# Kernel tuning notes

Measured on AMD Instinct MI355X. Metric: run time of the kernel, lower is better.

Reference implementation:

```python
import jax, jax.numpy as jnp
import numpy as np

IN, H, OUT = 128, 256, 128


def setup_inputs() -> dict:
    key = jax.random.key(0)
    ks = jax.random.split(key, 12)
    B, T = 32, 128
    s_in = 1.0 / np.sqrt(IN)
    s_h = 1.0 / np.sqrt(H)
    return {
        "x": jax.random.normal(ks[0], (B, T, IN), dtype=jnp.float32),
        "timespans": jax.random.uniform(ks[1], (B, T), dtype=jnp.float32),
        "tau_sys": jax.random.uniform(ks[2], (H,), dtype=jnp.float32) * 10.0 + 1.0,
        "sigma": jnp.ones((H,), dtype=jnp.float32) * 0.5,
        "W_A": jax.random.normal(ks[3], (H, H), dtype=jnp.float32) * s_h,
        "W_B": jax.random.normal(ks[4], (H, IN), dtype=jnp.float32) * s_in,
        "b_B": jax.random.normal(ks[5], (H,), dtype=jnp.float32) * s_in,
        "W_C": jax.random.normal(ks[6], (OUT, H), dtype=jnp.float32) * s_h,
        "b_C": jax.random.normal(ks[7], (OUT,), dtype=jnp.float32) * s_h,
        "W_ih": jax.random.normal(ks[8], (4 * H, IN), dtype=jnp.float32) * s_h,
        "W_hh": jax.random.normal(ks[9], (4 * H, H), dtype=jnp.float32) * s_h,
        "b_ih": jax.random.normal(ks[10], (4 * H,), dtype=jnp.float32) * s_h,
        "b_hh": jax.random.normal(ks[11], (4 * H,), dtype=jnp.float32) * s_h,
    }


def _lstm(x, W_ih, W_hh, b_ih, b_hh):
    # x: [B,T,IN] -> backbone_out: [B,T,H]; torch gate order i,f,g,o
    B = x.shape[0]
    xg = jnp.einsum("bti,gi->btg", x, W_ih) + b_ih  # precompute input contribution

    def step(carry, xg_t):
        h, c = carry
        gates = xg_t + h @ W_hh.T + b_hh
        i, f, g, o = jnp.split(gates, 4, axis=-1)
        c = jax.nn.sigmoid(f) * c + jax.nn.sigmoid(i) * jnp.tanh(g)
        h = jax.nn.sigmoid(o) * jnp.tanh(c)
        return (h, c), h

    h0 = jnp.zeros((B, H), dtype=x.dtype)
    c0 = jnp.zeros((B, H), dtype=x.dtype)
    _, hs = jax.lax.scan(step, (h0, c0), jnp.swapaxes(xg, 0, 1))
    return jnp.swapaxes(hs, 0, 1)  # [B,T,H]


def reference(x, timespans, tau_sys, sigma, W_A, W_B, b_B, W_C, b_C,
              W_ih, W_hh, b_ih, b_hh):
    B, T, _ = x.shape
    backbone_out = _lstm(x, W_ih, W_hh, b_ih, b_hh)  # [B,T,H]

    A_eff = W_A / tau_sys[None, :]        # [H,H] (divide columns, as in torch)
    I = jnp.eye(H, dtype=x.dtype)
    Bx = jnp.einsum("bti,hi->bth", x, W_B) + b_B  # precompute B(x_t) for all t

    def step(h, inp):
        x_t_Bx, bb_t, ts_t = inp  # [B,H], [B,H], [B]
        f_h = jnp.tanh(h / sigma)
        At = A_eff[None, :, :] * ts_t[:, None, None]            # [B,H,H]
        exp_At = I + At + 0.5 * jnp.einsum("bij,bjk->bik", At, At)
        h_new = jnp.einsum("bij,bj->bi", exp_At, h)
        drive = x_t_Bx + f_h @ W_A.T
        h_new = h_new + ts_t[:, None] * drive / tau_sys[None, :]
        h_new = h_new + bb_t
        y = h_new @ W_C.T + b_C
        return h_new, y

    h0 = jnp.zeros((B, H), dtype=x.dtype)
    xs = (jnp.swapaxes(Bx, 0, 1), jnp.swapaxes(backbone_out, 0, 1),
          jnp.swapaxes(timespans, 0, 1))
    _, ys = jax.lax.scan(step, h0, xs)
    return jnp.swapaxes(ys, 0, 1)  # [B,T,OUT]
```

## Files before the change

kernel.cpp:

```cpp
#include <hip/hip_runtime.h>
#include <math.h>

#define T_ 128

#define OFF_M2      0
#define OFF_WCOMBT  65536
#define OFF_BIAS    229376
#define OFF_WCT     230656
#define OFF_XG2     263424
#define OFF_BX2     4457728
#define OFF_HSEQ    5506304
#define OFF_HCSEQ   6554880

#define SENTB 0xFFFFFFFFu

__device__ __forceinline__ float sigm_f(float x) { return 1.0f / (1.0f + __expf(-x)); }
__device__ __forceinline__ float tanh_f(float x) { return 1.0f - 2.0f / (__expf(2.0f * x) + 1.0f); }

__device__ __forceinline__ unsigned long long aload_u64(const unsigned long long* p) {
  return __hip_atomic_load(p, __ATOMIC_RELAXED, __HIP_MEMORY_SCOPE_AGENT);
}
__device__ __forceinline__ void astore_f(float* p, float v) {
  __hip_atomic_store(p, v, __ATOMIC_RELAXED, __HIP_MEMORY_SCOPE_AGENT);
}
__device__ __forceinline__ bool bad_u64(unsigned long long v) {
  return (unsigned)v == SENTB || (unsigned)(v >> 32) == SENTB;
}

__global__ __launch_bounds__(256) void pack_kernel(
    const float* __restrict__ W_ih, const float* __restrict__ W_B,
    const float* __restrict__ b_ih, const float* __restrict__ b_hh,
    const float* __restrict__ b_B,  const float* __restrict__ W_C,
    float* __restrict__ ws) {
  int idx = blockIdx.x * 256 + threadIdx.x;
  if (idx < 163840) {
    int k = idx / 1280, c = idx - k * 1280;
    ws[OFF_WCOMBT + idx] = (c < 1024) ? W_ih[c * 128 + k] : W_B[(c - 1024) * 128 + k];
    return;
  }
  idx -= 163840;
  if (idx < 1280) {
    ws[OFF_BIAS + idx] = (idx < 1024) ? (b_ih[idx] + b_hh[idx]) : b_B[idx - 1024];
    return;
  }
  idx -= 1280;
  if (idx < 32768) {
    int k = idx >> 7, o = idx & 127;
    ws[OFF_WCT + idx] = W_C[o * 256 + k];
  }
}

__global__ __launch_bounds__(256) void m2_kernel(
    const float* __restrict__ W_A, const float* __restrict__ tau,
    float* __restrict__ M2) {
  __shared__ float adrow[256];
  const int i = blockIdx.x, k = threadIdx.x;
  const float itk = 1.0f / tau[k];
  adrow[k] = W_A[i * 256 + k] * itk;
  __syncthreads();
  float s = 0.f;
#pragma unroll 8
  for (int m = 0; m < 256; ++m)
    s = fmaf(adrow[m], W_A[m * 256 + k], s);
  M2[i * 256 + k] = s * itk;
}

__global__ __launch_bounds__(256) void xgt_kernel(
    const float* __restrict__ x, const float* __restrict__ WT,
    const float* __restrict__ bias, float* __restrict__ xg2,
    float* __restrict__ bx2) {
  __shared__ float xs[8 * 128];
  const int tid = threadIdx.x;
  const int rt = blockIdx.x, ct = blockIdx.y;
  ((float4*)xs)[tid] = ((const float4*)(x + rt * 1024))[tid];
  __syncthreads();
  const int r = tid >> 5, cg = tid & 31;
  const int c0 = ct * 256 + cg * 8;
  const float4* b4 = (const float4*)(bias + c0);
  float4 bA = b4[0], bB = b4[1];
  float a[8] = {bA.x, bA.y, bA.z, bA.w, bB.x, bB.y, bB.z, bB.w};
  const float4* xr4 = (const float4*)(xs + r * 128);
#pragma unroll 4
  for (int k4 = 0; k4 < 32; ++k4) {
    float4 xv = xr4[k4];
#define STEPB(kk, comp)                                                      \
    {                                                                        \
      const float4* w = (const float4*)(WT + (k4 * 4 + kk) * 1280 + c0);     \
      float4 wA = w[0], wB = w[1];                                           \
      a[0] = fmaf(wA.x, comp, a[0]); a[1] = fmaf(wA.y, comp, a[1]);          \
      a[2] = fmaf(wA.z, comp, a[2]); a[3] = fmaf(wA.w, comp, a[3]);          \
      a[4] = fmaf(wB.x, comp, a[4]); a[5] = fmaf(wB.y, comp, a[5]);          \
      a[6] = fmaf(wB.z, comp, a[6]); a[7] = fmaf(wB.w, comp, a[7]);          \
    }
    STEPB(0, xv.x) STEPB(1, xv.y) STEPB(2, xv.z) STEPB(3, xv.w)
#undef STEPB
  }
  const int row = rt * 8 + r;
  const int b = row >> 7, t = row & 127;
  if (ct < 4) {
    float* dst = xg2 + (size_t)(t * 32 + b) * 1024 + ct * 256 + cg * 8;
#pragma unroll
    for (int i = 0; i < 8; ++i) dst[i] = a[i];
  } else {
    float* dst = bx2 + (size_t)(t * 32 + b) * 256 + cg * 8;
#pragma unroll
    for (int i = 0; i < 8; ++i) dst[i] = a[i];
  }
}

__global__ __launch_bounds__(256) void recur_bp_kernel(
    const float* __restrict__ ts_all, const float* __restrict__ tau,
    const float* __restrict__ sigma, const float* __restrict__ W_hh,
    const float* __restrict__ W_A, const float* __restrict__ M2,
    const float* __restrict__ xg2, const float* __restrict__ bx2,
    float* __restrict__ hseq, float* __restrict__ hcseq) {
  const int tid = threadIdx.x;
  const int lane = tid & 63, w = tid >> 6;
  const unsigned long long* hsq  = (const unsigned long long*)hseq;
  const unsigned long long* hcsq = (const unsigned long long*)hcseq;

  __shared__ float h_s[2][256];
  __shared__ float q_s[2][768];

  if (blockIdx.x < 256) {
    const int b = blockIdx.x >> 3, cb = blockIdx.x & 7;
    const int p = lane >> 1, kh = lane & 1;
    const int gt = p >> 3, jj = p & 7;
    const int grow = gt * 256 + cb * 32 + 8 * w + jj;
    float4 wq[32];
    {
      const float4* src = (const float4*)(W_hh + grow * 256 + kh * 128);
#pragma unroll
      for (int k4 = 0; k4 < 32; ++k4) wq[k4] = src[k4];
    }
    float c_reg = 0.f;
    const int dcol = cb * 32 + 8 * w + lane;

    for (int t = 0; t < T_; ++t) {
      const int buf = t & 1;
      float xgi = 0.f, xgf = 0.f, xgg = 0.f, xgo = 0.f;
      if (lane < 8) {
        const float* xp = xg2 + (size_t)(t * 32 + b) * 1024 + dcol;
        xgi = xp[0]; xgf = xp[256]; xgg = xp[512]; xgo = xp[768];
      }
      if (t == 0) {
        if (tid < 128) ((float2*)h_s[0])[tid] = make_float2(0.f, 0.f);
      } else if (tid < 128) {
        const unsigned long long* pp = hsq + (size_t)((t - 1) * 32 + b) * 128 + tid;
        unsigned long long v = aload_u64(pp);
        int spins = 0;
        while (bad_u64(v)) {
          if (++spins > 16) __builtin_amdgcn_s_sleep(1);
          v = aload_u64(pp);
        }
        union { unsigned long long u; float2 f; } H; H.u = v;
        ((float2*)h_s[buf])[tid] = H.f;
      }
      __syncthreads();

      const float4* h4 = (const float4*)(&h_s[buf][0] + kh * 128);
      float s = 0.f;
#pragma unroll
      for (int k4 = 0; k4 < 32; ++k4) {
        const float4 wv = wq[k4], hv = h4[k4];
        s = fmaf(wv.x, hv.x, s); s = fmaf(wv.y, hv.y, s);
        s = fmaf(wv.z, hv.z, s); s = fmaf(wv.w, hv.w, s);
      }
      s += __shfl_xor(s, 1);
      const float gi = __shfl(s, 2 * lane);
      const float gf = __shfl(s, 2 * lane + 16);
      const float gg = __shfl(s, 2 * lane + 32);
      const float go = __shfl(s, 2 * lane + 48);
      if (lane < 8) {
        const float i_ = sigm_f(gi + xgi);
        const float f_ = sigm_f(gf + xgf);
        const float g_ = tanh_f(gg + xgg);
        const float o_ = sigm_f(go + xgo);
        c_reg = fmaf(f_, c_reg, i_ * g_);
        const float ht = o_ * tanh_f(c_reg);
        astore_f(hseq + (size_t)(t * 32 + b) * 256 + dcol, ht);
      }
    }
  } else {
    const int bix = blockIdx.x - 256;
    const int b = bix >> 3, cb = bix & 7;
    const int r = 8 * w + (lane >> 3), kq8 = lane & 7;
    const int ci = cb * 32 + r;
    const float it_i = 1.0f / tau[ci];
    float4 wcf[24];
#pragma unroll
    for (int i4 = 0; i4 < 24; ++i4) {
      float v[4];
#pragma unroll
      for (int e = 0; e < 4; ++e) {
        const int kp = 32 * i4 + 4 * kq8 + e;
        if (kp < 256)      v[e] = W_A[ci * 256 + kp] / tau[kp];
        else if (kp < 512) v[e] = W_A[ci * 256 + (kp - 256)] * it_i;
        else               v[e] = 0.5f * M2[ci * 256 + (kp - 512)];
      }
      wcf[i4] = make_float4(v[0], v[1], v[2], v[3]);
    }
    float2 isg2 = make_float2(0.f, 0.f);
    if (tid < 128) isg2 = make_float2(1.0f / sigma[2 * tid], 1.0f / sigma[2 * tid + 1]);
    const bool fin = (kq8 == 0);

    for (int t = 0; t < T_; ++t) {
      const int buf = t & 1;
      const float ts = ts_all[b * T_ + t];
      float bx_v = 0.f;
      if (fin) bx_v = bx2[(size_t)(t * 32 + b) * 256 + ci];

      if (t == 0) {
        if (tid < 128) {
          const float2 z = make_float2(0.f, 0.f);
          ((float2*)h_s[0])[tid] = z;
          float2* qrow = (float2*)q_s[0];
          qrow[tid] = z; qrow[128 + tid] = z; qrow[256 + tid] = z;
        }
      } else if (tid < 128) {
        const size_t base = (size_t)((t - 1) * 32 + b) * 128 + tid;
        const unsigned long long* pc = hcsq + base;
        const unsigned long long* ph = hsq + base;
        unsigned long long vc = aload_u64(pc);
        unsigned long long vh = aload_u64(ph);
        int spins = 0;
        while (bad_u64(vc) || bad_u64(vh)) {
          if (++spins > 16) __builtin_amdgcn_s_sleep(1);
          vc = aload_u64(pc);
          vh = aload_u64(ph);
        }
        union { unsigned long long u; float2 f; } C, H;
        C.u = vc; H.u = vh;
        const float2 hcv = make_float2(C.f.x + H.f.x, C.f.y + H.f.y);
        ((float2*)h_s[buf])[tid] = hcv;
        float2* qrow = (float2*)q_s[buf];
        qrow[tid]       = make_float2(ts * hcv.x, ts * hcv.y);
        qrow[128 + tid] = make_float2(ts * tanh_f(hcv.x * isg2.x),
                                      ts * tanh_f(hcv.y * isg2.y));
        qrow[256 + tid] = make_float2(ts * (ts * hcv.x), ts * (ts * hcv.y));
      }
      __syncthreads();

      const float4* q4 = (const float4*)q_s[buf];
      float s = 0.f;
#pragma unroll
      for (int i4 = 0; i4 < 24; ++i4) {
        const float4 wv = wcf[i4], qv = q4[i4 * 8 + kq8];
        s = fmaf(wv.x, qv.x, s); s = fmaf(wv.y, qv.y, s);
        s = fmaf(wv.z, qv.z, s); s = fmaf(wv.w, qv.w, s);
      }
      s += __shfl_xor(s, 1); s += __shfl_xor(s, 2); s += __shfl_xor(s, 4);
      if (fin) {
        const float hc_own = h_s[buf][ci];
        const float hn_p = hc_own + s + ts * bx_v * it_i;
        astore_f(hcseq + (size_t)(t * 32 + b) * 256 + ci, hn_p);
      }
    }
  }
}

__global__ __launch_bounds__(256) void out_kernel(
    const float* __restrict__ hc, const float* __restrict__ ht,
    const float* __restrict__ WCT, const float* __restrict__ bC,
    float* __restrict__ y) {
  __shared__ float hs[16 * 256];
  const int tid = threadIdx.x;
#pragma unroll
  for (int v = 0; v < 4; ++v) {
    const int flat = v * 256 + tid;
    const int r = flat >> 6, f4 = flat & 63;
    const int row = blockIdx.x * 16 + r;
    const int b = row >> 7, t = row & 127;
    const float4 a = ((const float4*)(hc + (size_t)(t * 32 + b) * 256))[f4];
    const float4 h = ((const float4*)(ht + (size_t)(t * 32 + b) * 256))[f4];
    ((float4*)hs)[flat] = make_float4(a.x + h.x, a.y + h.y, a.z + h.z, a.w + h.w);
  }
  __syncthreads();
  const int r = tid >> 4, cgg = tid & 15;
  const int c0 = cgg * 8;
  const float4* b4 = (const float4*)(bC + c0);
  float4 bA = b4[0], bB = b4[1];
  float a0 = bA.x, a1 = bA.y, a2 = bA.z, a3 = bA.w;
  float a4 = bB.x, a5 = bB.y, a6 = bB.z, a7 = bB.w;
  const float4* hr4 = (const float4*)(hs + r * 256);
#pragma unroll 4
  for (int k4 = 0; k4 < 64; ++k4) {
    float4 hv = hr4[k4];
#define STEPD(kk, comp)                                                     \
    {                                                                       \
      const float4* w = (const float4*)(WCT + (k4 * 4 + kk) * 128 + c0);    \
      float4 wA = w[0], wB = w[1];                                          \
      a0 = fmaf(wA.x, comp, a0); a1 = fmaf(wA.y, comp, a1);                 \
      a2 = fmaf(wA.z, comp, a2); a3 = fmaf(wA.w, comp, a3);                 \
      a4 = fmaf(wB.x, comp, a4); a5 = fmaf(wB.y, comp, a5);                 \
      a6 = fmaf(wB.z, comp, a6); a7 = fmaf(wB.w, comp, a7);                 \
    }
    STEPD(0, hv.x) STEPD(1, hv.y) STEPD(2, hv.z) STEPD(3, hv.w)
#undef STEPD
  }
  const int row = blockIdx.x * 16 + r;
  float4* dst = (float4*)(y + (size_t)row * 128 + c0);
  dst[0] = make_float4(a0, a1, a2, a3);
  dst[1] = make_float4(a4, a5, a6, a7);
}

extern "C" void kernel_launch(void* const* d_in, const int* in_sizes, int n_in,
                              void* d_out, int out_size, void* d_ws, size_t ws_size,
                              hipStream_t stream) {
  const float* x     = (const float*)d_in[0];
  const float* tspan = (const float*)d_in[1];
  const float* tau   = (const float*)d_in[2];
  const float* sigma = (const float*)d_in[3];
  const float* W_A   = (const float*)d_in[4];
  const float* W_B   = (const float*)d_in[5];
  const float* b_B   = (const float*)d_in[6];
  const float* W_C   = (const float*)d_in[7];
  const float* b_C   = (const float*)d_in[8];
  const float* W_ih  = (const float*)d_in[9];
  const float* W_hh  = (const float*)d_in[10];
  const float* b_ih  = (const float*)d_in[11];
  const float* b_hh  = (const float*)d_in[12];
  float* ws = (float*)d_ws;
  float* y = (float*)d_out;

  (void)hipMemsetAsync(ws + OFF_HSEQ, 0xFF, (size_t)2 * 1048576 * sizeof(float), stream);
  pack_kernel<<<774, 256, 0, stream>>>(W_ih, W_B, b_ih, b_hh, b_B, W_C, ws);
  m2_kernel<<<256, 256, 0, stream>>>(W_A, tau, ws + OFF_M2);
  xgt_kernel<<<dim3(512, 5), 256, 0, stream>>>(x, ws + OFF_WCOMBT, ws + OFF_BIAS,
                                               ws + OFF_XG2, ws + OFF_BX2);
  recur_bp_kernel<<<512, 256, 0, stream>>>(
      tspan, tau, sigma, W_hh, W_A, ws + OFF_M2, ws + OFF_XG2, ws + OFF_BX2,
      ws + OFF_HSEQ, ws + OFF_HCSEQ);
  out_kernel<<<256, 256, 0, stream>>>(ws + OFF_HCSEQ, ws + OFF_HSEQ,
                                      ws + OFF_WCT, b_C, y);
}
```

Before: 428.3 us.

## Fuse LSTM input projection into recurrent kernel and merge prep kernels

Drops the precomputed xg buffer (about 16 MB written and then read back). The LSTM recurrent blocks now hold the W_ih slice in registers and compute the input contribution each step from x staged in shared memory. The pack, M2 and memset launches become one prep kernel that also writes the sentinel fill, and the Bx projection becomes its own smaller kernel. The cost is more per-step FMA work on the serial critical path and higher register pressure (wq plus wx) under launch_bounds(256,2).

```diff
diff --git a/kernel.cpp b/kernel.cpp
--- a/kernel.cpp
+++ b/kernel.cpp
@@ -7,7 +7,6 @@
 #define OFF_WCOMBT  65536
 #define OFF_BIAS    229376
 #define OFF_WCT     230656
-#define OFF_XG2     263424
 #define OFF_BX2     4457728
 #define OFF_HSEQ    5506304
 #define OFF_HCSEQ   6554880
@@ -27,55 +26,51 @@
   return (unsigned)v == SENTB || (unsigned)(v >> 32) == SENTB;
 }
 
-__global__ __launch_bounds__(256) void pack_kernel(
-    const float* __restrict__ W_ih, const float* __restrict__ W_B,
-    const float* __restrict__ b_ih, const float* __restrict__ b_hh,
-    const float* __restrict__ b_B,  const float* __restrict__ W_C,
-    float* __restrict__ ws) {
-  int idx = blockIdx.x * 256 + threadIdx.x;
-  if (idx < 163840) {
-    int k = idx / 1280, c = idx - k * 1280;
-    ws[OFF_WCOMBT + idx] = (c < 1024) ? W_ih[c * 128 + k] : W_B[(c - 1024) * 128 + k];
-    return;
-  }
-  idx -= 163840;
-  if (idx < 1280) {
-    ws[OFF_BIAS + idx] = (idx < 1024) ? (b_ih[idx] + b_hh[idx]) : b_B[idx - 1024];
-    return;
-  }
-  idx -= 1280;
-  if (idx < 32768) {
-    int k = idx >> 7, o = idx & 127;
+__global__ __launch_bounds__(256) void prep_kernel(
+    const float* __restrict__ W_B, const float* __restrict__ b_B,
+    const float* __restrict__ W_C, const float* __restrict__ W_A,
+    const float* __restrict__ tau, float* __restrict__ ws) {
+  __shared__ float adrow[256];
+  const int blk = blockIdx.x, tid = threadIdx.x;
+  if (blk < 128) {
+    const int idx = blk * 256 + tid;
+    const int k = idx >> 8, c = idx & 255;
+    ws[OFF_WCOMBT + k * 1280 + 1024 + c] = W_B[c * 128 + k];
+  } else if (blk == 128) {
+    ws[OFF_BIAS + 1024 + tid] = b_B[tid];
+  } else if (blk < 257) {
+    const int idx = (blk - 129) * 256 + tid;
+    const int k = idx >> 7, o = idx & 127;
     ws[OFF_WCT + idx] = W_C[o * 256 + k];
-  }
-}
-
-__global__ __launch_bounds__(256) void m2_kernel(
-    const float* __restrict__ W_A, const float* __restrict__ tau,
-    float* __restrict__ M2) {
-  __shared__ float adrow[256];
-  const int i = blockIdx.x, k = threadIdx.x;
-  const float itk = 1.0f / tau[k];
-  adrow[k] = W_A[i * 256 + k] * itk;
-  __syncthreads();
-  float s = 0.f;
+  } else if (blk < 513) {
+    const int i = blk - 257, k = tid;
+    const float itk = 1.0f / tau[k];
+    adrow[k] = W_A[i * 256 + k] * itk;
+    __syncthreads();
+    float s = 0.f;
 #pragma unroll 8
-  for (int m = 0; m < 256; ++m)
-    s = fmaf(adrow[m], W_A[m * 256 + k], s);
-  M2[i * 256 + k] = s * itk;
-}
-
-__global__ __launch_bounds__(256) void xgt_kernel(
+    for (int m = 0; m < 256; ++m)
+      s = fmaf(adrow[m], W_A[m * 256 + k], s);
+    ws[OFF_M2 + i * 256 + k] = s * itk;
+  } else {
+    uint4* dst = (uint4*)(ws + OFF_HSEQ);
+    const uint4 sv = make_uint4(SENTB, SENTB, SENTB, SENTB);
+    const int tg = (blk - 513) * 256 + tid;
+#pragma unroll
+    for (int i = 0; i < 16; ++i) dst[tg + i * 32768] = sv;
+  }
+}
+
+__global__ __launch_bounds__(256) void bx_kernel(
     const float* __restrict__ x, const float* __restrict__ WT,
-    const float* __restrict__ bias, float* __restrict__ xg2,
-    float* __restrict__ bx2) {
+    const float* __restrict__ bias, float* __restrict__ bx2) {
   __shared__ float xs[8 * 128];
   const int tid = threadIdx.x;
-  const int rt = blockIdx.x, ct = blockIdx.y;
+  const int rt = blockIdx.x;
   ((float4*)xs)[tid] = ((const float4*)(x + rt * 1024))[tid];
   __syncthreads();
   const int r = tid >> 5, cg = tid & 31;
-  const int c0 = ct * 256 + cg * 8;
+  const int c0 = 1024 + cg * 8;
   const float4* b4 = (const float4*)(bias + c0);
   float4 bA = b4[0], bB = b4[1];
   float a[8] = {bA.x, bA.y, bA.z, bA.w, bB.x, bB.y, bB.z, bB.w};
@@ -97,22 +92,18 @@
   }
   const int row = rt * 8 + r;
   const int b = row >> 7, t = row & 127;
-  if (ct < 4) {
-    float* dst = xg2 + (size_t)(t * 32 + b) * 1024 + ct * 256 + cg * 8;
-#pragma unroll
-    for (int i = 0; i < 8; ++i) dst[i] = a[i];
-  } else {
-    float* dst = bx2 + (size_t)(t * 32 + b) * 256 + cg * 8;
-#pragma unroll
-    for (int i = 0; i < 8; ++i) dst[i] = a[i];
-  }
-}
-
-__global__ __launch_bounds__(256) void recur_bp_kernel(
-    const float* __restrict__ ts_all, const float* __restrict__ tau,
-    const float* __restrict__ sigma, const float* __restrict__ W_hh,
+  float* dst = bx2 + (size_t)(t * 32 + b) * 256 + cg * 8;
+#pragma unroll
+  for (int i = 0; i < 8; ++i) dst[i] = a[i];
+}
+
+__global__ __launch_bounds__(256, 2) void recur_bp_kernel(
+    const float* __restrict__ x, const float* __restrict__ ts_all,
+    const float* __restrict__ tau, const float* __restrict__ sigma,
+    const float* __restrict__ W_hh, const float* __restrict__ W_ih,
+    const float* __restrict__ b_ih, const float* __restrict__ b_hh,
     const float* __restrict__ W_A, const float* __restrict__ M2,
-    const float* __restrict__ xg2, const float* __restrict__ bx2,
+    const float* __restrict__ bx2,
     float* __restrict__ hseq, float* __restrict__ hcseq) {
   const int tid = threadIdx.x;
   const int lane = tid & 63, w = tid >> 6;
@@ -121,6 +112,7 @@
 
   __shared__ float h_s[2][256];
   __shared__ float q_s[2][768];
+  __shared__ float xs_s[2][128];
 
   if (blockIdx.x < 256) {
     const int b = blockIdx.x >> 3, cb = blockIdx.x & 7;
@@ -133,16 +125,26 @@
 #pragma unroll
       for (int k4 = 0; k4 < 32; ++k4) wq[k4] = src[k4];
     }
+    float4 wx[16];
+    {
+      const float4* src = (const float4*)(W_ih + grow * 128 + kh * 64);
+#pragma unroll
+      for (int k4 = 0; k4 < 16; ++k4) wx[k4] = src[k4];
+    }
     float c_reg = 0.f;
     const int dcol = cb * 32 + 8 * w + lane;
+    float bias4[4] = {0.f, 0.f, 0.f, 0.f};
+    if (lane < 8) {
+#pragma unroll
+      for (int g = 0; g < 4; ++g)
+        bias4[g] = b_ih[g * 256 + dcol] + b_hh[g * 256 + dcol];
+    }
 
     for (int t = 0; t < T_; ++t) {
       const int buf = t & 1;
-      float xgi = 0.f, xgf = 0.f, xgg = 0.f, xgo = 0.f;
-      if (lane < 8) {
-        const float* xp = xg2 + (size_t)(t * 32 + b) * 1024 + dcol;
-        xgi = xp[0]; xgf = xp[256]; xgg = xp[512]; xgo = xp[768];
-      }
+      if (tid >= 128 && tid < 160)
+        ((float4*)xs_s[buf])[tid - 128] =
+            ((const float4*)(x + ((size_t)b * T_ + t) * 128))[tid - 128];
       if (t == 0) {
         if (tid < 128) ((float2*)h_s[0])[tid] = make_float2(0.f, 0.f);
       } else if (tid < 128) {
@@ -159,12 +161,19 @@
       __syncthreads();
 
       const float4* h4 = (const float4*)(&h_s[buf][0] + kh * 128);
+      const float4* x4 = (const float4*)(&xs_s[buf][0] + kh * 64);
       float s = 0.f;
 #pragma unroll
       for (int k4 = 0; k4 < 32; ++k4) {
         const float4 wv = wq[k4], hv = h4[k4];
         s = fmaf(wv.x, hv.x, s); s = fmaf(wv.y, hv.y, s);
         s = fmaf(wv.z, hv.z, s); s = fmaf(wv.w, hv.w, s);
+      }
+#pragma unroll
+      for (int k4 = 0; k4 < 16; ++k4) {
+        const float4 wv = wx[k4], xv = x4[k4];
+        s = fmaf(wv.x, xv.x, s); s = fmaf(wv.y, xv.y, s);
+        s = fmaf(wv.z, xv.z, s); s = fmaf(wv.w, xv.w, s);
       }
       s += __shfl_xor(s, 1);
       const float gi = __shfl(s, 2 * lane);
@@ -172,10 +181,10 @@
       const float gg = __shfl(s, 2 * lane + 32);
       const float go = __shfl(s, 2 * lane + 48);
       if (lane < 8) {
-        const float i_ = sigm_f(gi + xgi);
-        const float f_ = sigm_f(gf + xgf);
-        const float g_ = tanh_f(gg + xgg);
-        const float o_ = sigm_f(go + xgo);
+        const float i_ = sigm_f(gi + bias4[0]);
+        const float f_ = sigm_f(gf + bias4[1]);
+        const float g_ = tanh_f(gg + bias4[2]);
+        const float o_ = sigm_f(go + bias4[3]);
         c_reg = fmaf(f_, c_reg, i_ * g_);
         const float ht = o_ * tanh_f(c_reg);
         astore_f(hseq + (size_t)(t * 32 + b) * 256 + dcol, ht);
@@ -323,14 +332,12 @@
   float* ws = (float*)d_ws;
   float* y = (float*)d_out;
 
-  (void)hipMemsetAsync(ws + OFF_HSEQ, 0xFF, (size_t)2 * 1048576 * sizeof(float), stream);
-  pack_kernel<<<774, 256, 0, stream>>>(W_ih, W_B, b_ih, b_hh, b_B, W_C, ws);
-  m2_kernel<<<256, 256, 0, stream>>>(W_A, tau, ws + OFF_M2);
-  xgt_kernel<<<dim3(512, 5), 256, 0, stream>>>(x, ws + OFF_WCOMBT, ws + OFF_BIAS,
-                                               ws + OFF_XG2, ws + OFF_BX2);
+  prep_kernel<<<641, 256, 0, stream>>>(W_B, b_B, W_C, W_A, tau, ws);
+  bx_kernel<<<512, 256, 0, stream>>>(x, ws + OFF_WCOMBT, ws + OFF_BIAS,
+                                     ws + OFF_BX2);
   recur_bp_kernel<<<512, 256, 0, stream>>>(
-      tspan, tau, sigma, W_hh, W_A, ws + OFF_M2, ws + OFF_XG2, ws + OFF_BX2,
-      ws + OFF_HSEQ, ws + OFF_HCSEQ);
+      x, tspan, tau, sigma, W_hh, W_ih, b_ih, b_hh, W_A, ws + OFF_M2,
+      ws + OFF_BX2, ws + OFF_HSEQ, ws + OFF_HCSEQ);
   out_kernel<<<256, 256, 0, stream>>>(ws + OFF_HCSEQ, ws + OFF_HSEQ,
                                       ws + OFF_WCT, b_C, y);
 }
```

Result: no change. 434.7 us (+1.5%).

## Split recurrence across twice as many blocks and fuse prep kernels with sentinel fill

Applied to the files above, without the earlier changes.

Each recurrence block now owns 16 hidden columns instead of 32, which doubles the grid to 1024 blocks and halves the per-thread register weight slices. Dot products are split across 4 or 16 lanes and reduced with extra shuffles. The goal is shorter per-step critical paths and more parallelism, at the cost of more blocks polling the shared sequence buffers. Separately, the pack, M2 and sentinel-memset launches are merged into one prep kernel to cut launch overhead. The persistent spin-wait design needs all 1024 blocks co-resident, which risks deadlock if they do not fit, so launch_bounds(256,4) is added.

```diff
diff --git a/kernel.cpp b/kernel.cpp
--- a/kernel.cpp
+++ b/kernel.cpp
@@ -27,42 +27,45 @@
   return (unsigned)v == SENTB || (unsigned)(v >> 32) == SENTB;
 }
 
-__global__ __launch_bounds__(256) void pack_kernel(
+__global__ __launch_bounds__(256) void prep_kernel(
     const float* __restrict__ W_ih, const float* __restrict__ W_B,
     const float* __restrict__ b_ih, const float* __restrict__ b_hh,
     const float* __restrict__ b_B,  const float* __restrict__ W_C,
+    const float* __restrict__ W_A,  const float* __restrict__ tau,
     float* __restrict__ ws) {
-  int idx = blockIdx.x * 256 + threadIdx.x;
-  if (idx < 163840) {
-    int k = idx / 1280, c = idx - k * 1280;
+  __shared__ float adrow[256];
+  const int blk = blockIdx.x, tid = threadIdx.x;
+  if (blk < 640) {
+    const int idx = blk * 256 + tid;
+    const int k = idx / 1280, c = idx - k * 1280;
     ws[OFF_WCOMBT + idx] = (c < 1024) ? W_ih[c * 128 + k] : W_B[(c - 1024) * 128 + k];
-    return;
-  }
-  idx -= 163840;
-  if (idx < 1280) {
-    ws[OFF_BIAS + idx] = (idx < 1024) ? (b_ih[idx] + b_hh[idx]) : b_B[idx - 1024];
-    return;
-  }
-  idx -= 1280;
-  if (idx < 32768) {
-    int k = idx >> 7, o = idx & 127;
+  } else if (blk == 640) {
+#pragma unroll
+    for (int i = 0; i < 5; ++i) {
+      const int id = i * 256 + tid;
+      ws[OFF_BIAS + id] = (id < 1024) ? (b_ih[id] + b_hh[id]) : b_B[id - 1024];
+    }
+  } else if (blk < 769) {
+    const int idx = (blk - 641) * 256 + tid;
+    const int k = idx >> 7, o = idx & 127;
     ws[OFF_WCT + idx] = W_C[o * 256 + k];
-  }
-}
-
-__global__ __launch_bounds__(256) void m2_kernel(
-    const float* __restrict__ W_A, const float* __restrict__ tau,
-    float* __restrict__ M2) {
-  __shared__ float adrow[256];
-  const int i = blockIdx.x, k = threadIdx.x;
-  const float itk = 1.0f / tau[k];
-  adrow[k] = W_A[i * 256 + k] * itk;
-  __syncthreads();
-  float s = 0.f;
+  } else if (blk < 1025) {
+    const int i = blk - 769, k = tid;
+    const float itk = 1.0f / tau[k];
+    adrow[k] = W_A[i * 256 + k] * itk;
+    __syncthreads();
+    float s = 0.f;
 #pragma unroll 8
-  for (int m = 0; m < 256; ++m)
-    s = fmaf(adrow[m], W_A[m * 256 + k], s);
-  M2[i * 256 + k] = s * itk;
+    for (int m = 0; m < 256; ++m)
+      s = fmaf(adrow[m], W_A[m * 256 + k], s);
+    ws[OFF_M2 + i * 256 + k] = s * itk;
+  } else {
+    uint4* dst = (uint4*)(ws + OFF_HSEQ);
+    const uint4 sv = make_uint4(SENTB, SENTB, SENTB, SENTB);
+    const int tg = (blk - 1025) * 256 + tid;
+#pragma unroll
+    for (int i = 0; i < 16; ++i) dst[tg + i * 32768] = sv;
+  }
 }
 
 __global__ __launch_bounds__(256) void xgt_kernel(
@@ -108,7 +111,7 @@
   }
 }
 
-__global__ __launch_bounds__(256) void recur_bp_kernel(
+__global__ __launch_bounds__(256, 4) void recur_bp_kernel(
     const float* __restrict__ ts_all, const float* __restrict__ tau,
     const float* __restrict__ sigma, const float* __restrict__ W_hh,
     const float* __restrict__ W_A, const float* __restrict__ M2,
@@ -122,24 +125,24 @@
   __shared__ float h_s[2][256];
   __shared__ float q_s[2][768];
 
-  if (blockIdx.x < 256) {
-    const int b = blockIdx.x >> 3, cb = blockIdx.x & 7;
-    const int p = lane >> 1, kh = lane & 1;
-    const int gt = p >> 3, jj = p & 7;
-    const int grow = gt * 256 + cb * 32 + 8 * w + jj;
-    float4 wq[32];
+  if (blockIdx.x < 512) {
+    const int b = blockIdx.x >> 4, cb16 = blockIdx.x & 15;
+    const int d_in = lane >> 4, gt = (lane >> 2) & 3, kq = lane & 3;
+    const int dim = cb16 * 16 + 4 * w + d_in;
+    const int grow = gt * 256 + dim;
+    float4 wq[16];
     {
-      const float4* src = (const float4*)(W_hh + grow * 256 + kh * 128);
-#pragma unroll
-      for (int k4 = 0; k4 < 32; ++k4) wq[k4] = src[k4];
+      const float4* src = (const float4*)(W_hh + grow * 256);
+#pragma unroll
+      for (int i4 = 0; i4 < 16; ++i4) wq[i4] = src[i4 * 4 + kq];
     }
     float c_reg = 0.f;
-    const int dcol = cb * 32 + 8 * w + lane;
+    const int dcol = cb16 * 16 + 4 * w + (lane >> 4);
 
     for (int t = 0; t < T_; ++t) {
       const int buf = t & 1;
       float xgi = 0.f, xgf = 0.f, xgg = 0.f, xgo = 0.f;
-      if (lane < 8) {
+      if ((lane & 15) == 0) {
         const float* xp = xg2 + (size_t)(t * 32 + b) * 1024 + dcol;
         xgi = xp[0]; xgf = xp[256]; xgg = xp[512]; xgo = xp[768];
       }
@@ -158,20 +161,21 @@
       }
       __syncthreads();
 
-      const float4* h4 = (const float4*)(&h_s[buf][0] + kh * 128);
+      const float4* h4 = (const float4*)h_s[buf];
       float s = 0.f;
 #pragma unroll
-      for (int k4 = 0; k4 < 32; ++k4) {
-        const float4 wv = wq[k4], hv = h4[k4];
+      for (int i4 = 0; i4 < 16; ++i4) {
+        const float4 wv = wq[i4], hv = h4[i4 * 4 + kq];
         s = fmaf(wv.x, hv.x, s); s = fmaf(wv.y, hv.y, s);
         s = fmaf(wv.z, hv.z, s); s = fmaf(wv.w, hv.w, s);
       }
-      s += __shfl_xor(s, 1);
-      const float gi = __shfl(s, 2 * lane);
-      const float gf = __shfl(s, 2 * lane + 16);
-      const float gg = __shfl(s, 2 * lane + 32);
-      const float go = __shfl(s, 2 * lane + 48);
-      if (lane < 8) {
+      s += __shfl_xor(s, 1); s += __shfl_xor(s, 2);
+      const int base = lane & 48;
+      const float gi = __shfl(s, base);
+      const float gf = __shfl(s, base + 4);
+      const float gg = __shfl(s, base + 8);
+      const float go = __shfl(s, base + 12);
+      if ((lane & 15) == 0) {
         const float i_ = sigm_f(gi + xgi);
         const float f_ = sigm_f(gf + xgf);
         const float g_ = tanh_f(gg + xgg);
@@ -182,18 +186,18 @@
       }
     }
   } else {
-    const int bix = blockIdx.x - 256;
-    const int b = bix >> 3, cb = bix & 7;
-    const int r = 8 * w + (lane >> 3), kq8 = lane & 7;
-    const int ci = cb * 32 + r;
+    const int bix = blockIdx.x - 512;
+    const int b = bix >> 4, cb16 = bix & 15;
+    const int r_in = lane >> 4, kq16 = lane & 15;
+    const int ci = cb16 * 16 + 4 * w + r_in;
     const float it_i = 1.0f / tau[ci];
-    float4 wcf[24];
-#pragma unroll
-    for (int i4 = 0; i4 < 24; ++i4) {
+    float4 wcf[12];
+#pragma unroll
+    for (int i4 = 0; i4 < 12; ++i4) {
       float v[4];
 #pragma unroll
       for (int e = 0; e < 4; ++e) {
-        const int kp = 32 * i4 + 4 * kq8 + e;
+        const int kp = (i4 * 16 + kq16) * 4 + e;
         if (kp < 256)      v[e] = W_A[ci * 256 + kp] / tau[kp];
         else if (kp < 512) v[e] = W_A[ci * 256 + (kp - 256)] * it_i;
         else               v[e] = 0.5f * M2[ci * 256 + (kp - 512)];
@@ -202,7 +206,7 @@
     }
     float2 isg2 = make_float2(0.f, 0.f);
     if (tid < 128) isg2 = make_float2(1.0f / sigma[2 * tid], 1.0f / sigma[2 * tid + 1]);
-    const bool fin = (kq8 == 0);
+    const bool fin = (kq16 == 0);
 
     for (int t = 0; t < T_; ++t) {
       const int buf = t & 1;
@@ -244,12 +248,13 @@
       const float4* q4 = (const float4*)q_s[buf];
       float s = 0.f;
 #pragma unroll
-      for (int i4 = 0; i4 < 24; ++i4) {
-        const float4 wv = wcf[i4], qv = q4[i4 * 8 + kq8];
+      for (int i4 = 0; i4 < 12; ++i4) {
+        const float4 wv = wcf[i4], qv = q4[i4 * 16 + kq16];
         s = fmaf(wv.x, qv.x, s); s = fmaf(wv.y, qv.y, s);
         s = fmaf(wv.z, qv.z, s); s = fmaf(wv.w, qv.w, s);
       }
-      s += __shfl_xor(s, 1); s += __shfl_xor(s, 2); s += __shfl_xor(s, 4);
+      s += __shfl_xor(s, 1); s += __shfl_xor(s, 2);
+      s += __shfl_xor(s, 4); s += __shfl_xor(s, 8);
       if (fin) {
         const float hc_own = h_s[buf][ci];
         const float hn_p = hc_own + s + ts * bx_v * it_i;
@@ -323,12 +328,11 @@
   float* ws = (float*)d_ws;
   float* y = (float*)d_out;
 
-  (void)hipMemsetAsync(ws + OFF_HSEQ, 0xFF, (size_t)2 * 1048576 * sizeof(float), stream);
-  pack_kernel<<<774, 256, 0, stream>>>(W_ih, W_B, b_ih, b_hh, b_B, W_C, ws);
-  m2_kernel<<<256, 256, 0, stream>>>(W_A, tau, ws + OFF_M2);
+  prep_kernel<<<1153, 256, 0, stream>>>(W_ih, W_B, b_ih, b_hh, b_B, W_C,
+                                        W_A, tau, ws);
   xgt_kernel<<<dim3(512, 5), 256, 0, stream>>>(x, ws + OFF_WCOMBT, ws + OFF_BIAS,
                                                ws + OFF_XG2, ws + OFF_BX2);
-  recur_bp_kernel<<<512, 256, 0, stream>>>(
+  recur_bp_kernel<<<1024, 256, 0, stream>>>(
       tspan, tau, sigma, W_hh, W_A, ws + OFF_M2, ws + OFF_XG2, ws + OFF_BX2,
       ws + OFF_HSEQ, ws + OFF_HCSEQ);
   out_kernel<<<256, 256, 0, stream>>>(ws + OFF_HCSEQ, ws + OFF_HSEQ,
```

After: 466.5 us. 1.09x slower.
